# Performance work log

Hardware: AMD Instinct MI355X
Metric: run time of the kernel (lower is better)

## Reference

```python
import jax, jax.numpy as jnp
import numpy as np

L, B, H, S, V, D = 2, 128, 1024, 512, 32000, 64
W_SCALE = 0.02

def setup_inputs() -> dict:
    key = jax.random.key(0)
    ks = jax.random.split(key, 17)
    f = lambda k, shape: jax.random.normal(k, shape, dtype=jnp.float32)
    return {
        "input_ids": jax.random.randint(ks[0], (1, B), 0, V),
        "h": f(ks[1], (L, B, H)),
        "c": f(ks[2], (L, B, H)),
        "h_s": f(ks[3], (S, B, H)),
        "emb": f(ks[4], (V, H)),
        "W_pt": f(ks[5], (H, H)) * W_SCALE,
        "b_pt": f(ks[6], (H,)) * W_SCALE,
        "v_pt": f(ks[7], (H,)) * W_SCALE,
        "b_v": f(ks[8], (1,)) * W_SCALE,
        "W_a": f(ks[9], (H, H)) * W_SCALE,
        "b_a": f(ks[10], (1,)) * W_SCALE,
        "W_ih": f(ks[11], (L, 4 * H, H)) * W_SCALE,
        "W_hh": f(ks[12], (L, 4 * H, H)) * W_SCALE,
        "b_ih": f(ks[13], (L, 4 * H)) * W_SCALE,
        "b_hh": f(ks[14], (L, 4 * H)) * W_SCALE,
        "W_out": f(ks[15], (V, H)) * W_SCALE,
        "b_out": f(ks[16], (V,)) * W_SCALE,
    }


def reference(input_ids, h, c, h_s, emb, W_pt, b_pt, v_pt, b_v, W_a, b_a,
              W_ih, W_hh, b_ih, b_hh, W_out, b_out):
    S_len = h_s.shape[0]
    x_emb = emb[input_ids]                     # [1, B, H]
    h_top = h[-1]                              # [B, H] top-layer decoder state
    # predicted alignment position p_t = S * sigmoid(v . tanh(W h + b))
    p_t = S_len * jax.nn.sigmoid(jnp.tanh(h_top @ W_pt.T + b_pt) @ v_pt + b_v[0])  # [B]
    s = jnp.clip(jnp.round(p_t).astype(jnp.int32), D, S_len - 1 - D)               # [B]
    # gather local window h_s[s-D : s+D+1] per batch element
    idx = s[:, None] + jnp.arange(-D, D + 1)    # [B, 2D+1]
    h_s_b = jnp.transpose(h_s, (1, 0, 2))       # [B, S, H]
    h_loc = jnp.take_along_axis(h_s_b, idx[:, :, None], axis=1)  # [B, 2D+1, H]
    # bilinear score h_t^T W_a h_s_j per window position
    scores = jnp.einsum('bh,hk,bjk->bj', h_top, W_a, h_loc) + b_a[0]  # [B, 2D+1]
    sigma2 = (D / 2.0) ** 2
    gauss = jnp.exp(-((idx.astype(p_t.dtype) - p_t[:, None]) ** 2) / (2.0 * sigma2))
    a_t = jax.nn.softmax(scores, axis=-1) * gauss                      # [B, 2D+1]
    context = jnp.einsum('bj,bjh->bh', a_t, h_loc)                     # [B, H]
    # inject context into the LSTM hidden state, then run one step
    h_in = h + context[None]                    # [L, B, H]
    x = x_emb[0]                                # [B, H]
    hs, cs = [], []
    for l in range(h.shape[0]):
        gates = x @ W_ih[l].T + b_ih[l] + h_in[l] @ W_hh[l].T + b_hh[l]
        i, f, g, o = jnp.split(gates, 4, axis=-1)
        c_new = jax.nn.sigmoid(f) * c[l] + jax.nn.sigmoid(i) * jnp.tanh(g)
        h_new = jax.nn.sigmoid(o) * jnp.tanh(c_new)
        hs.append(h_new)
        cs.append(c_new)
        x = h_new
    h_out = jnp.stack(hs)                       # [L, B, H]
    c_out = jnp.stack(cs)                       # [L, B, H]
    logits = jax.nn.log_softmax(x @ W_out.T + b_out, axis=-1)  # [B, V]
    return logits, h_out, c_out, context, s
```

## Files before the change

### kernel.cpp

```cpp
#include <hip/hip_runtime.h>
#include <hip/hip_bf16.h>
#include <math.h>

typedef __bf16 bf16_8 __attribute__((ext_vector_type(8)));
typedef __bf16 bf16_4 __attribute__((ext_vector_type(4)));
typedef float  f32x4  __attribute__((ext_vector_type(4)));

static __device__ __forceinline__ float sigmoidf_(float x){ return 1.0f/(1.0f + expf(-x)); }

#define BB 128
#define HH 1024
#define SS 512
#define VV 32000

#define OFF_A0    0u
#define OFF_A1    524288u
#define OFF_ALOG  1048576u
#define OFF_AH    1310720u
#define OFF_AM    1572864u
#define OFF_AL    1835008u
#define OFF_WAT   2097152u
#define OFF_Q     6291456u
#define OFF_Z     6815744u
#define OFF_PT    7340032u
#define OFF_SI    7340544u
#define OFF_SC    7341056u
#define OFF_G0P   7408640u
#define OFF_G1P   15797248u
#define OFF_PMAX  24185856u
#define OFF_PSUM  24313856u

__global__ void k_prep_all(const float* __restrict__ W_a, float* __restrict__ WaT,
                           const int* __restrict__ ids, const float* __restrict__ emb,
                           const float* __restrict__ h, const float* __restrict__ b_pt,
                           __bf16* __restrict__ A0, __bf16* __restrict__ Ah,
                           __bf16* __restrict__ Am, __bf16* __restrict__ Al,
                           float* __restrict__ z, float* __restrict__ q){
  __shared__ float tsm[32][33];
  int blk = blockIdx.x, t = threadIdx.x;
  if (blk < 1024){
    int kt = blk & 31, nt = blk >> 5;
    int c = t & 31, r0 = t >> 5;
    #pragma unroll
    for (int i = 0; i < 4; ++i){
      int r = r0 + 8*i;
      tsm[r][c] = W_a[(size_t)(kt*32 + r)*HH + nt*32 + c];
    }
    __syncthreads();
    #pragma unroll
    for (int i = 0; i < 4; ++i){
      int r = r0 + 8*i;
      WaT[(size_t)(nt*32 + r)*HH + kt*32 + c] = tsm[c][r];
    }
  } else {
    int b = blk - 1024, c = t*4;
    int tok = ids[b];
    f32x4 e = *(const f32x4*)(emb + (size_t)tok*HH + c);
    bf16_4 e4;
    #pragma unroll
    for (int i=0;i<4;i++) e4[i] = (__bf16)e[i];
    *(bf16_4*)(A0 + (size_t)b*2048 + c) = e4;
    f32x4 x = *(const f32x4*)(h + (size_t)BB*HH + (size_t)b*HH + c);
    bf16_4 hi4, mi4, lo4;
    #pragma unroll
    for (int i=0;i<4;i++){
      float v = x[i];
      __bf16 bh = (__bf16)v; float r1 = v - (float)bh;
      __bf16 bm = (__bf16)r1; float r2 = r1 - (float)bm;
      hi4[i]=bh; mi4[i]=bm; lo4[i]=(__bf16)r2;
    }
    *(bf16_4*)(Ah + (size_t)b*HH + c) = hi4;
    *(bf16_4*)(Am + (size_t)b*HH + c) = mi4;
    *(bf16_4*)(Al + (size_t)b*HH + c) = lo4;
    *(f32x4*)(z + (size_t)b*HH + c) = *(const f32x4*)(b_pt + c);
    *(f32x4*)(q + (size_t)b*HH + c) = f32x4{0.f,0.f,0.f,0.f};
  }
}

template<int PREC>
__device__ __forceinline__ void gemm_small(
    char* smem,
    const __bf16* __restrict__ Ah, const __bf16* __restrict__ Am, const __bf16* __restrict__ Al,
    int lda, const float* __restrict__ B1, int K,
    float* __restrict__ C, int N, int xblk, int ysplit)
{
  constexpr int NS   = PREC;
  constexpr int BK   = 32;
  constexpr int KG   = BK/8;
  constexpr int TILE = 128*BK*2;
  constexpr int UPT  = (128*KG)/256;
  char* sA = smem;
  char* sB = smem + NS*TILE;

  const int t = threadIdx.x;
  const int lane = t & 63, wave = t >> 6;
  const int wm = wave >> 1, wn = wave & 1;
  const int quad = lane >> 4, ln = lane & 15;
  const int nblock = xblk * 128;
  const int kchunk = K / ysplit;
  const int kstart = blockIdx.y * kchunk;
  const int kend = kstart + kchunk;

  f32x4 acc[4][4];
  #pragma unroll
  for (int i=0;i<4;i++)
    #pragma unroll
    for (int j=0;j<4;j++) acc[i][j] = f32x4{0.f,0.f,0.f,0.f};

  for (int k0 = kstart; k0 < kend; k0 += BK){
    #pragma unroll
    for (int i = 0; i < UPT; ++i){
      int u = t + 256*i;
      int row = u / KG, kg = u % KG;
      int sl = row*(BK*2) + (((kg ^ (row & (KG-1)))) << 4);
      *(uint4*)(sA + sl) = *(const uint4*)(Ah + (size_t)row*lda + k0 + kg*8);
      if constexpr (PREC >= 2)
        *(uint4*)(sA + TILE + sl) = *(const uint4*)(Am + (size_t)row*lda + k0 + kg*8);
      if constexpr (PREC >= 3)
        *(uint4*)(sA + 2*TILE + sl) = *(const uint4*)(Al + (size_t)row*lda + k0 + kg*8);
      int ng = nblock + row;
      const float* src = B1 + (size_t)ng*K + k0 + kg*8;
      f32x4 x0 = *(const f32x4*)(src);
      f32x4 x1 = *(const f32x4*)(src + 4);
      bf16_8 hi, mi, lo;
      #pragma unroll
      for (int qv=0;qv<8;qv++){
        float v = (qv<4) ? x0[qv] : x1[qv-4];
        __bf16 bh = (__bf16)v;
        hi[qv] = bh;
        float r1 = v - (float)bh;
        __bf16 bm = (__bf16)r1;
        mi[qv] = bm;
        lo[qv] = (__bf16)(r1 - (float)bm);
      }
      *(bf16_8*)(sB + sl) = hi;
      if constexpr (PREC >= 2) *(bf16_8*)(sB + TILE + sl) = mi;
      if constexpr (PREC >= 3) *(bf16_8*)(sB + 2*TILE + sl) = lo;
    }
    __syncthreads();
    {
      bf16_8 af[NS][4], bfr[NS][4];
      #pragma unroll
      for (int mt=0; mt<4; ++mt){
        int row = wm*64 + mt*16 + ln;
        int kg = quad;
        int sl = row*(BK*2) + (((kg ^ (row & (KG-1)))) << 4);
        #pragma unroll
        for (int s=0;s<NS;s++) af[s][mt] = *(const bf16_8*)(sA + s*TILE + sl);
      }
      #pragma unroll
      for (int nt=0; nt<4; ++nt){
        int row = wn*64 + nt*16 + ln;
        int kg = quad;
        int sl = row*(BK*2) + (((kg ^ (row & (KG-1)))) << 4);
        #pragma unroll
        for (int s=0;s<NS;s++) bfr[s][nt] = *(const bf16_8*)(sB + s*TILE + sl);
      }
      #pragma unroll
      for (int mt=0; mt<4; ++mt)
        #pragma unroll
        for (int nt=0; nt<4; ++nt){
          acc[mt][nt] = __builtin_amdgcn_mfma_f32_16x16x32_bf16(af[0][mt], bfr[0][nt], acc[mt][nt], 0,0,0);
          if constexpr (PREC >= 2){
            acc[mt][nt] = __builtin_amdgcn_mfma_f32_16x16x32_bf16(af[0][mt], bfr[1][nt], acc[mt][nt], 0,0,0);
            acc[mt][nt] = __builtin_amdgcn_mfma_f32_16x16x32_bf16(af[1][mt], bfr[0][nt], acc[mt][nt], 0,0,0);
          }
          if constexpr (PREC >= 3){
            acc[mt][nt] = __builtin_amdgcn_mfma_f32_16x16x32_bf16(af[0][mt], bfr[2][nt], acc[mt][nt], 0,0,0);
            acc[mt][nt] = __builtin_amdgcn_mfma_f32_16x16x32_bf16(af[1][mt], bfr[1][nt], acc[mt][nt], 0,0,0);
            acc[mt][nt] = __builtin_amdgcn_mfma_f32_16x16x32_bf16(af[2][mt], bfr[0][nt], acc[mt][nt], 0,0,0);
          }
        }
    }
    __syncthreads();
  }

  #pragma unroll
  for (int nt=0; nt<4; ++nt){
    int n = nblock + wn*64 + nt*16 + ln;
    #pragma unroll
    for (int mt=0; mt<4; ++mt){
      int m0 = wm*64 + mt*16 + quad*4;
      #pragma unroll
      for (int r=0;r<4;++r)
        atomicAdd(C + (size_t)(m0 + r)*N + n, acc[mt][nt][r]);
    }
  }
}

__global__ __launch_bounds__(256) void k_qz(
    const __bf16* __restrict__ Ah, const __bf16* __restrict__ Am, const __bf16* __restrict__ Al,
    const float* __restrict__ WaT, const float* __restrict__ Wpt,
    float* __restrict__ q, float* __restrict__ z)
{
  __shared__ __align__(16) char smem[49152];
  if (blockIdx.x < 8)
    gemm_small<2>(smem, Ah, Am, nullptr, 1024, WaT, 1024, q, 1024, blockIdx.x, 4);
  else
    gemm_small<3>(smem, Ah, Am, Al, 1024, Wpt, 1024, z, 1024, blockIdx.x - 8, 4);
}

template<int PREC, int EPI>
__global__ __launch_bounds__(256) void k_gemm(
    const __bf16* __restrict__ Ah, const __bf16* __restrict__ Am, const __bf16* __restrict__ Al,
    int lda,
    const float* __restrict__ B1, const float* __restrict__ B2, int K1, int K2,
    const float* __restrict__ bias,
    float* __restrict__ C, int N,
    float* __restrict__ Pmax, float* __restrict__ Psum)
{
  constexpr int BK  = 64;
  constexpr int KG  = BK/8;
  constexpr int TILE = 128*BK*2;
  constexpr int UPT = (128*KG)/256;
  __shared__ __align__(16) char smem[2*TILE];
  char* sA = smem;
  char* sB = smem + TILE;

  const int t = threadIdx.x;
  const int lane = t & 63, wave = t >> 6;
  const int wm = wave >> 1, wn = wave & 1;
  const int quad = lane >> 4, ln = lane & 15;
  const int nblock = blockIdx.x * 128;
  const int K = K1 + K2;
  const int kchunk = K / gridDim.y;
  const int kstart = blockIdx.y * kchunk;
  const int kend = kstart + kchunk;

  f32x4 acc[4][4];
  #pragma unroll
  for (int i=0;i<4;i++)
    #pragma unroll
    for (int j=0;j<4;j++) acc[i][j] = f32x4{0.f,0.f,0.f,0.f};

  uint4 aR[UPT]; f32x4 bR[UPT][2];
  auto issue = [&](int k0){
    #pragma unroll
    for (int i=0;i<UPT;++i){
      int u = t + 256*i, row = u/KG, kg = u%KG;
      aR[i] = *(const uint4*)(Ah + (size_t)row*lda + k0 + kg*8);
      int ng = nblock + row;
      const float* src = (k0 < K1) ? (B1 + (size_t)ng*K1 + k0 + kg*8)
                                   : (B2 + (size_t)ng*K2 + (k0 - K1) + kg*8);
      bR[i][0] = *(const f32x4*)(src);
      bR[i][1] = *(const f32x4*)(src + 4);
    }
  };
  issue(kstart);
  for (int k0 = kstart; k0 < kend; k0 += BK){
    __syncthreads();
    #pragma unroll
    for (int i=0;i<UPT;++i){
      int u = t + 256*i, row = u/KG, kg = u%KG;
      int sl = row*(BK*2) + (((kg ^ (row & (KG-1)))) << 4);
      *(uint4*)(sA + sl) = aR[i];
      bf16_8 hi;
      #pragma unroll
      for (int qv=0;qv<8;++qv) hi[qv] = (__bf16)((qv<4) ? bR[i][0][qv] : bR[i][1][qv-4]);
      *(bf16_8*)(sB + sl) = hi;
    }
    __syncthreads();
    if (k0 + BK < kend) issue(k0 + BK);
    #pragma unroll
    for (int ks = 0; ks < BK/32; ++ks){
      bf16_8 af[4], bfr[4];
      #pragma unroll
      for (int mt=0; mt<4; ++mt){
        int row = wm*64 + mt*16 + ln;
        int kg = ks*4 + quad;
        int sl = row*(BK*2) + (((kg ^ (row & (KG-1)))) << 4);
        af[mt] = *(const bf16_8*)(sA + sl);
      }
      #pragma unroll
      for (int nt=0; nt<4; ++nt){
        int row = wn*64 + nt*16 + ln;
        int kg = ks*4 + quad;
        int sl = row*(BK*2) + (((kg ^ (row & (KG-1)))) << 4);
        bfr[nt] = *(const bf16_8*)(sB + sl);
      }
      #pragma unroll
      for (int mt=0; mt<4; ++mt)
        #pragma unroll
        for (int nt=0; nt<4; ++nt)
          acc[mt][nt] = __builtin_amdgcn_mfma_f32_16x16x32_bf16(af[mt], bfr[nt], acc[mt][nt], 0,0,0);
    }
  }

  if constexpr (EPI == 4){
    float* Cp = C + (size_t)blockIdx.y * 128 * N;
    #pragma unroll
    for (int nt=0; nt<4; ++nt){
      int n = nblock + wn*64 + nt*16 + ln;
      #pragma unroll
      for (int mt=0; mt<4; ++mt){
        int m0 = wm*64 + mt*16 + quad*4;
        #pragma unroll
        for (int r=0;r<4;++r)
          Cp[(size_t)(m0 + r)*N + n] = acc[mt][nt][r];
      }
    }
  } else if constexpr (EPI == 2){
    __syncthreads();
    float* redm = (float*)smem;
    float* reds = (float*)smem + 256;
    float rmax[16];
    #pragma unroll
    for (int mt=0; mt<4; ++mt)
      #pragma unroll
      for (int r=0;r<4;++r){
        float m4 = -1e30f;
        #pragma unroll
        for (int nt=0;nt<4;++nt){
          int n = nblock + wn*64 + nt*16 + ln;
          m4 = fmaxf(m4, acc[mt][nt][r] + bias[n]);
        }
        #pragma unroll
        for (int m=1;m<16;m<<=1) m4 = fmaxf(m4, __shfl_xor(m4, m));
        rmax[mt*4+r] = m4;
      }
    if (ln == 0){
      #pragma unroll
      for (int mt=0;mt<4;++mt)
        #pragma unroll
        for (int r=0;r<4;++r)
          redm[wn*128 + wm*64 + mt*16 + quad*4 + r] = rmax[mt*4+r];
    }
    __syncthreads();
    #pragma unroll
    for (int mt=0; mt<4; ++mt)
      #pragma unroll
      for (int r=0;r<4;++r){
        int row = wm*64 + mt*16 + quad*4 + r;
        float M = fmaxf(redm[row], redm[128 + row]);
        float s4 = 0.f;
        #pragma unroll
        for (int nt=0;nt<4;++nt){
          int n = nblock + wn*64 + nt*16 + ln;
          float v = acc[mt][nt][r] + bias[n];
          C[(size_t)row*N + n] = v;
          s4 += expf(v - M);
        }
        #pragma unroll
        for (int m=1;m<16;m<<=1) s4 += __shfl_xor(s4, m);
        if (ln == 0) reds[wn*128 + row] = s4;
      }
    __syncthreads();
    if (wn == 0 && ln == 0){
      #pragma unroll
      for (int mt=0;mt<4;++mt)
        #pragma unroll
        for (int r=0;r<4;++r){
          int row = wm*64 + mt*16 + quad*4 + r;
          float M = fmaxf(redm[row], redm[128 + row]);
          Pmax[(size_t)blockIdx.x*128 + row] = M;
          Psum[(size_t)blockIdx.x*128 + row] = reds[row] + reds[128 + row];
        }
    }
  }
}

__global__ __launch_bounds__(256) void k_scores(
    const float* __restrict__ z, const float* __restrict__ v_pt, const float* __restrict__ b_v,
    const float* __restrict__ q, const float* __restrict__ h_s,
    const float* __restrict__ b_a,
    float* __restrict__ sc, float* __restrict__ p_t, int* __restrict__ s_i,
    float* __restrict__ out_s)
{
  __shared__ float red[4];
  __shared__ float sh[2];
  int b = blockIdx.x, t = threadIdx.x;
  {
    f32x4 zv = *(const f32x4*)(z + (size_t)b*HH + t*4);
    f32x4 vv = *(const f32x4*)(v_pt + t*4);
    float ps = tanhf(zv[0])*vv[0] + tanhf(zv[1])*vv[1] + tanhf(zv[2])*vv[2] + tanhf(zv[3])*vv[3];
    #pragma unroll
    for (int m=1;m<64;m<<=1) ps += __shfl_xor(ps, m);
    if ((t&63)==0) red[t>>6] = ps;
    __syncthreads();
    if (t == 0){
      float tot = red[0]+red[1]+red[2]+red[3] + b_v[0];
      float p = (float)SS * sigmoidf_(tot);
      float sf = rintf(p);
      sf = fminf(fmaxf(sf, 64.0f), 447.0f);
      sh[0] = p; sh[1] = sf;
      if (blockIdx.y == 0){ p_t[b] = p; s_i[b] = (int)sf; out_s[b] = sf; }
    }
    __syncthreads();
  }
  int si = (int)sh[1];
  int jj = blockIdx.y*4 + (t >> 6);
  if (jj >= 129) return;
  int lane = t & 63;
  int pos = si - 64 + jj;
  const float* row = h_s + ((size_t)pos*BB + b)*HH;
  const float* qb  = q + (size_t)b*HH;
  f32x4 a = f32x4{0.f,0.f,0.f,0.f};
  #pragma unroll
  for (int c = lane*4; c < HH; c += 256){
    f32x4 r4 = *(const f32x4*)(row + c);
    f32x4 q4 = *(const f32x4*)(qb + c);
    a += r4*q4;
  }
  float sdot = a[0]+a[1]+a[2]+a[3];
  #pragma unroll
  for (int m=1;m<64;m<<=1) sdot += __shfl_xor(sdot, m);
  if (lane == 0) sc[b*132 + jj] = sdot + b_a[0];
}

__global__ __launch_bounds__(256) void k_context(
    const float* __restrict__ sc, const int* __restrict__ s_i, const float* __restrict__ p_t,
    const float* __restrict__ h_s, const float* __restrict__ h,
    float* __restrict__ ctx_out, __bf16* __restrict__ A0, __bf16* __restrict__ A1){
  __shared__ float sat[132];
  __shared__ float sctx[4][512];
  __shared__ int spos;
  int bb = blockIdx.x;
  int b = bb >> 1, half = bb & 1;
  int t = threadIdx.x, w = t >> 6, l = t & 63;
  if (w == 0){
    const float* scb = sc + b*132;
    float mx = -1e30f;
    for (int j=l; j<129; j+=64) mx = fmaxf(mx, scb[j]);
    #pragma unroll
    for (int m=1;m<64;m<<=1) mx = fmaxf(mx, __shfl_xor(mx, m));
    float sum = 0.f;
    for (int j=l; j<129; j+=64) sum += expf(scb[j] - mx);
    #pragma unroll
    for (int m=1;m<64;m<<=1) sum += __shfl_xor(sum, m);
    float inv = 1.0f/sum;
    float pt = p_t[b];
    int si = s_i[b];
    if (l == 0) spos = si - 64;
    float s0 = (float)(si - 64);
    for (int j=l; j<129; j+=64){
      float e = expf(scb[j]-mx)*inv;
      float d = (s0 + (float)j) - pt;
      sat[j] = e * expf(-(d*d) * (1.0f/2048.0f));
    }
  }
  __syncthreads();
  int pos0 = spos;
  int jstart = (w == 0) ? 0 : (33 + 32*(w-1));
  int jcnt   = (w == 0) ? 33 : 32;
  const float* base = h_s + ((size_t)pos0*BB + b)*HH + half*512;
  f32x4 acc0 = f32x4{0.f,0.f,0.f,0.f};
  f32x4 acc1 = f32x4{0.f,0.f,0.f,0.f};
  for (int j = jstart; j < jstart + jcnt; ++j){
    const float* row = base + (size_t)j*BB*HH;
    float aj = sat[j];
    acc0 += *(const f32x4*)(row + l*4) * aj;
    acc1 += *(const f32x4*)(row + 256 + l*4) * aj;
  }
  *(f32x4*)(&sctx[w][l*4])       = acc0;
  *(f32x4*)(&sctx[w][256 + l*4]) = acc1;
  __syncthreads();
  if (t < 128){
    int c = t*4;
    f32x4 v = *(f32x4*)(&sctx[0][c]) + *(f32x4*)(&sctx[1][c])
            + *(f32x4*)(&sctx[2][c]) + *(f32x4*)(&sctx[3][c]);
    int gc = half*512 + c;
    *(f32x4*)(ctx_out + (size_t)b*HH + gc) = v;
    f32x4 h0 = *(const f32x4*)(h + (size_t)b*HH + gc) + v;
    f32x4 h1 = *(const f32x4*)(h + (size_t)BB*HH + (size_t)b*HH + gc) + v;
    bf16_4 v0, v1;
    #pragma unroll
    for (int i=0;i<4;i++){ v0[i]=(__bf16)h0[i]; v1[i]=(__bf16)h1[i]; }
    *(bf16_4*)(A0 + (size_t)b*2048 + 1024 + gc) = v0;
    *(bf16_4*)(A1 + (size_t)b*2048 + 1024 + gc) = v1;
  }
}

__global__ void k_cell(const float* __restrict__ part,
                       const float* __restrict__ bih, const float* __restrict__ bhh,
                       const float* __restrict__ c_in,
                       float* __restrict__ h_out, float* __restrict__ c_out,
                       __bf16* __restrict__ Anext, int strideNext){
  int g = blockIdx.x*256 + threadIdx.x;
  int b = g >> 10, hc = g & 1023;
  float ig = bih[hc]        + bhh[hc];
  float fg = bih[1024 + hc] + bhh[1024 + hc];
  float gg = bih[2048 + hc] + bhh[2048 + hc];
  float og = bih[3072 + hc] + bhh[3072 + hc];
  #pragma unroll
  for (int y = 0; y < 4; ++y){
    const float* gb = part + ((size_t)y*BB + b)*4096;
    ig += gb[hc]; fg += gb[1024+hc]; gg += gb[2048+hc]; og += gb[3072+hc];
  }
  float cn = sigmoidf_(fg)*c_in[g] + sigmoidf_(ig)*tanhf(gg);
  float hn = sigmoidf_(og)*tanhf(cn);
  c_out[g] = cn; h_out[g] = hn;
  Anext[(size_t)b*strideNext + hc] = (__bf16)hn;
}

__global__ void k_lsesub(const float* __restrict__ Pmax, const float* __restrict__ Psum,
                         float* __restrict__ out){
  int b = blockIdx.y, l = threadIdx.x;
  float M = -1e30f;
  for (int i=l; i<250; i+=64) M = fmaxf(M, Pmax[(size_t)i*128 + b]);
  #pragma unroll
  for (int m=1;m<64;m<<=1) M = fmaxf(M, __shfl_xor(M, m));
  float s = 0.f;
  for (int i=l; i<250; i+=64) s += Psum[(size_t)i*128 + b] * expf(Pmax[(size_t)i*128 + b] - M);
  #pragma unroll
  for (int m=1;m<64;m<<=1) s += __shfl_xor(s, m);
  float L = M + logf(s);
  int i = blockIdx.x*256 + l*4;
  f32x4 v = *(f32x4*)(out + (size_t)b*VV + i);
  v[0]-=L; v[1]-=L; v[2]-=L; v[3]-=L;
  *(f32x4*)(out + (size_t)b*VV + i) = v;
}

extern "C" void kernel_launch(void* const* d_in, const int* in_sizes, int n_in,
                              void* d_out, int out_size, void* d_ws, size_t ws_size,
                              hipStream_t stream){
  const int*   ids   = (const int*)d_in[0];
  const float* h     = (const float*)d_in[1];
  const float* c     = (const float*)d_in[2];
  const float* h_s   = (const float*)d_in[3];
  const float* emb   = (const float*)d_in[4];
  const float* W_pt  = (const float*)d_in[5];
  const float* b_pt  = (const float*)d_in[6];
  const float* v_pt  = (const float*)d_in[7];
  const float* b_v   = (const float*)d_in[8];
  const float* W_a   = (const float*)d_in[9];
  const float* b_a   = (const float*)d_in[10];
  const float* W_ih  = (const float*)d_in[11];
  const float* W_hh  = (const float*)d_in[12];
  const float* b_ih  = (const float*)d_in[13];
  const float* b_hh  = (const float*)d_in[14];
  const float* W_out = (const float*)d_in[15];
  const float* b_out = (const float*)d_in[16];

  char* ws = (char*)d_ws;
  __bf16* A0   = (__bf16*)(ws + OFF_A0);
  __bf16* A1   = (__bf16*)(ws + OFF_A1);
  __bf16* Alog = (__bf16*)(ws + OFF_ALOG);
  __bf16* Ah   = (__bf16*)(ws + OFF_AH);
  __bf16* Am   = (__bf16*)(ws + OFF_AM);
  __bf16* Al   = (__bf16*)(ws + OFF_AL);
  float* WaT   = (float*)(ws + OFF_WAT);
  float* q     = (float*)(ws + OFF_Q);
  float* z     = (float*)(ws + OFF_Z);
  float* p_t   = (float*)(ws + OFF_PT);
  int*   s_i   = (int*)  (ws + OFF_SI);
  float* sc    = (float*)(ws + OFF_SC);
  float* g0p   = (float*)(ws + OFF_G0P);
  float* g1p   = (float*)(ws + OFF_G1P);
  float* Pmax  = (float*)(ws + OFF_PMAX);
  float* Psum  = (float*)(ws + OFF_PSUM);

  float* out        = (float*)d_out;
  float* out_logits = out;
  float* out_h      = out + 4096000;
  float* out_c      = out + 4358144;
  float* out_ctx    = out + 4620288;
  float* out_s      = out + 4751360;

  k_prep_all<<<1152, 256, 0, stream>>>(W_a, WaT, ids, emb, h, b_pt, A0, Ah, Am, Al, z, q);
  k_qz<<<dim3(16,4), 256, 0, stream>>>(Ah, Am, Al, WaT, W_pt, q, z);
  k_scores<<<dim3(128,33), 256, 0, stream>>>(z, v_pt, b_v, q, h_s, b_a, sc, p_t, s_i, out_s);
  k_context<<<256, 256, 0, stream>>>(sc, s_i, p_t, h_s, h, out_ctx, A0, A1);
  k_gemm<1,4><<<dim3(32,4), 256, 0, stream>>>(A0, nullptr, nullptr, 2048, W_ih, W_hh, 1024, 1024,
                                              nullptr, g0p, 4096, nullptr, nullptr);
  k_cell<<<512, 256, 0, stream>>>(g0p, b_ih, b_hh, c, out_h, out_c, A1, 2048);
  k_gemm<1,4><<<dim3(32,4), 256, 0, stream>>>(A1, nullptr, nullptr, 2048, W_ih + 4194304, W_hh + 4194304,
                                              1024, 1024, nullptr, g1p, 4096, nullptr, nullptr);
  k_cell<<<512, 256, 0, stream>>>(g1p, b_ih + 4096, b_hh + 4096, c + 131072,
                                  out_h + 131072, out_c + 131072, Alog, 1024);
  k_gemm<1,2><<<dim3(250,1), 256, 0, stream>>>(Alog, nullptr, nullptr, 1024, W_out, nullptr, 1024, 0,
                                               b_out, out_logits, 32000, Pmax, Psum);
  k_lsesub<<<dim3(125,128), 64, 0, stream>>>(Pmax, Psum, out_logits);
}
```

Baseline: 651.5 us.

## Double split-K for gate GEMMs and qz, narrow logits tiles to 64 columns

The gate GEMMs and the q/z projection now split K eight ways instead of four, and the cell kernel sums eight partials. Workspace offsets grow to hold the larger partial buffers. The logits GEMM becomes a dedicated kernel with 64-wide N tiles, launching 500 blocks instead of 250, and each wave does its own row max/sum reduction with no shared-memory cross-wave step. The aim is to fill more compute units on the MI355X for these weight-bandwidth-bound GEMMs, at the cost of more partial-sum traffic and a longer LSE reduction.

```diff
diff --git a/kernel.cpp b/kernel.cpp
--- a/kernel.cpp
+++ b/kernel.cpp
@@ -26,9 +26,9 @@
 #define OFF_SI    7340544u
 #define OFF_SC    7341056u
 #define OFF_G0P   7408640u
-#define OFF_G1P   15797248u
-#define OFF_PMAX  24185856u
-#define OFF_PSUM  24313856u
+#define OFF_G1P   24185856u
+#define OFF_PMAX  40963072u
+#define OFF_PSUM  41225216u
 
 __global__ void k_prep_all(const float* __restrict__ W_a, float* __restrict__ WaT,
                            const int* __restrict__ ids, const float* __restrict__ emb,
@@ -195,19 +195,15 @@
 {
   __shared__ __align__(16) char smem[49152];
   if (blockIdx.x < 8)
-    gemm_small<2>(smem, Ah, Am, nullptr, 1024, WaT, 1024, q, 1024, blockIdx.x, 4);
+    gemm_small<2>(smem, Ah, Am, nullptr, 1024, WaT, 1024, q, 1024, blockIdx.x, 8);
   else
-    gemm_small<3>(smem, Ah, Am, Al, 1024, Wpt, 1024, z, 1024, blockIdx.x - 8, 4);
-}
-
-template<int PREC, int EPI>
-__global__ __launch_bounds__(256) void k_gemm(
-    const __bf16* __restrict__ Ah, const __bf16* __restrict__ Am, const __bf16* __restrict__ Al,
-    int lda,
-    const float* __restrict__ B1, const float* __restrict__ B2, int K1, int K2,
-    const float* __restrict__ bias,
-    float* __restrict__ C, int N,
-    float* __restrict__ Pmax, float* __restrict__ Psum)
+    gemm_small<3>(smem, Ah, Am, Al, 1024, Wpt, 1024, z, 1024, blockIdx.x - 8, 8);
+}
+
+__global__ __launch_bounds__(256) void k_gates(
+    const __bf16* __restrict__ Ain, int lda,
+    const float* __restrict__ B1, const float* __restrict__ B2, int K1,
+    float* __restrict__ C, int N)
 {
   constexpr int BK  = 64;
   constexpr int KG  = BK/8;
@@ -222,7 +218,7 @@
   const int wm = wave >> 1, wn = wave & 1;
   const int quad = lane >> 4, ln = lane & 15;
   const int nblock = blockIdx.x * 128;
-  const int K = K1 + K2;
+  const int K = 2*K1;
   const int kchunk = K / gridDim.y;
   const int kstart = blockIdx.y * kchunk;
   const int kend = kstart + kchunk;
@@ -238,10 +234,10 @@
     #pragma unroll
     for (int i=0;i<UPT;++i){
       int u = t + 256*i, row = u/KG, kg = u%KG;
-      aR[i] = *(const uint4*)(Ah + (size_t)row*lda + k0 + kg*8);
+      aR[i] = *(const uint4*)(Ain + (size_t)row*lda + k0 + kg*8);
       int ng = nblock + row;
       const float* src = (k0 < K1) ? (B1 + (size_t)ng*K1 + k0 + kg*8)
-                                   : (B2 + (size_t)ng*K2 + (k0 - K1) + kg*8);
+                                   : (B2 + (size_t)ng*K1 + (k0 - K1) + kg*8);
       bR[i][0] = *(const f32x4*)(src);
       bR[i][1] = *(const f32x4*)(src + 4);
     }
@@ -286,77 +282,131 @@
     }
   }
 
-  if constexpr (EPI == 4){
-    float* Cp = C + (size_t)blockIdx.y * 128 * N;
-    #pragma unroll
-    for (int nt=0; nt<4; ++nt){
-      int n = nblock + wn*64 + nt*16 + ln;
-      #pragma unroll
-      for (int mt=0; mt<4; ++mt){
-        int m0 = wm*64 + mt*16 + quad*4;
+  float* Cp = C + (size_t)blockIdx.y * 128 * N;
+  #pragma unroll
+  for (int nt=0; nt<4; ++nt){
+    int n = nblock + wn*64 + nt*16 + ln;
+    #pragma unroll
+    for (int mt=0; mt<4; ++mt){
+      int m0 = wm*64 + mt*16 + quad*4;
+      #pragma unroll
+      for (int r=0;r<4;++r)
+        Cp[(size_t)(m0 + r)*N + n] = acc[mt][nt][r];
+    }
+  }
+}
+
+__global__ __launch_bounds__(256) void k_logits(
+    const __bf16* __restrict__ A, const float* __restrict__ Wout,
+    const float* __restrict__ bias, float* __restrict__ C,
+    float* __restrict__ Pmax, float* __restrict__ Psum)
+{
+  constexpr int BK = 64, KG = 8;
+  constexpr int ATILE = 128*BK*2;
+  constexpr int BTILE = 64*BK*2;
+  __shared__ __align__(16) char smem[ATILE + BTILE];
+  char* sA = smem;
+  char* sB = smem + ATILE;
+
+  const int t = threadIdx.x;
+  const int lane = t & 63, wave = t >> 6;
+  const int quad = lane >> 4, ln = lane & 15;
+  const int nblock = blockIdx.x * 64;
+
+  f32x4 acc[2][4];
+  #pragma unroll
+  for (int i=0;i<2;i++)
+    #pragma unroll
+    for (int j=0;j<4;j++) acc[i][j] = f32x4{0.f,0.f,0.f,0.f};
+
+  uint4 aR[4]; f32x4 bR[2][2];
+  auto issue = [&](int k0){
+    #pragma unroll
+    for (int i=0;i<4;++i){
+      int u = t + 256*i, row = u >> 3, kg = u & 7;
+      aR[i] = *(const uint4*)(A + (size_t)row*HH + k0 + kg*8);
+    }
+    #pragma unroll
+    for (int i=0;i<2;++i){
+      int u = t + 256*i, row = u >> 3, kg = u & 7;
+      const float* src = Wout + (size_t)(nblock + row)*HH + k0 + kg*8;
+      bR[i][0] = *(const f32x4*)(src);
+      bR[i][1] = *(const f32x4*)(src + 4);
+    }
+  };
+  issue(0);
+  for (int k0 = 0; k0 < HH; k0 += BK){
+    __syncthreads();
+    #pragma unroll
+    for (int i=0;i<4;++i){
+      int u = t + 256*i, row = u >> 3, kg = u & 7;
+      int sl = row*(BK*2) + ((kg ^ (row & 7)) << 4);
+      *(uint4*)(sA + sl) = aR[i];
+    }
+    #pragma unroll
+    for (int i=0;i<2;++i){
+      int u = t + 256*i, row = u >> 3, kg = u & 7;
+      int sl = row*(BK*2) + ((kg ^ (row & 7)) << 4);
+      bf16_8 hi;
+      #pragma unroll
+      for (int qv=0;qv<8;++qv) hi[qv] = (__bf16)((qv<4) ? bR[i][0][qv] : bR[i][1][qv-4]);
+      *(bf16_8*)(sB + sl) = hi;
+    }
+    __syncthreads();
+    if (k0 + BK < HH) issue(k0 + BK);
+    #pragma unroll
+    for (int ks = 0; ks < BK/32; ++ks){
+      bf16_8 af[2], bfr[4];
+      #pragma unroll
+      for (int mt=0; mt<2; ++mt){
+        int row = wave*32 + mt*16 + ln;
+        int kg = ks*4 + quad;
+        int sl = row*(BK*2) + ((kg ^ (row & 7)) << 4);
+        af[mt] = *(const bf16_8*)(sA + sl);
+      }
+      #pragma unroll
+      for (int nt=0; nt<4; ++nt){
+        int row = nt*16 + ln;
+        int kg = ks*4 + quad;
+        int sl = row*(BK*2) + ((kg ^ (row & 7)) << 4);
+        bfr[nt] = *(const bf16_8*)(sB + sl);
+      }
+      #pragma unroll
+      for (int mt=0; mt<2; ++mt)
         #pragma unroll
-        for (int r=0;r<4;++r)
-          Cp[(size_t)(m0 + r)*N + n] = acc[mt][nt][r];
-      }
-    }
-  } else if constexpr (EPI == 2){
-    __syncthreads();
-    float* redm = (float*)smem;
-    float* reds = (float*)smem + 256;
-    float rmax[16];
-    #pragma unroll
-    for (int mt=0; mt<4; ++mt)
-      #pragma unroll
-      for (int r=0;r<4;++r){
-        float m4 = -1e30f;
-        #pragma unroll
-        for (int nt=0;nt<4;++nt){
-          int n = nblock + wn*64 + nt*16 + ln;
-          m4 = fmaxf(m4, acc[mt][nt][r] + bias[n]);
-        }
-        #pragma unroll
-        for (int m=1;m<16;m<<=1) m4 = fmaxf(m4, __shfl_xor(m4, m));
-        rmax[mt*4+r] = m4;
-      }
-    if (ln == 0){
-      #pragma unroll
-      for (int mt=0;mt<4;++mt)
-        #pragma unroll
-        for (int r=0;r<4;++r)
-          redm[wn*128 + wm*64 + mt*16 + quad*4 + r] = rmax[mt*4+r];
-    }
-    __syncthreads();
-    #pragma unroll
-    for (int mt=0; mt<4; ++mt)
-      #pragma unroll
-      for (int r=0;r<4;++r){
-        int row = wm*64 + mt*16 + quad*4 + r;
-        float M = fmaxf(redm[row], redm[128 + row]);
-        float s4 = 0.f;
-        #pragma unroll
-        for (int nt=0;nt<4;++nt){
-          int n = nblock + wn*64 + nt*16 + ln;
-          float v = acc[mt][nt][r] + bias[n];
-          C[(size_t)row*N + n] = v;
-          s4 += expf(v - M);
-        }
-        #pragma unroll
-        for (int m=1;m<16;m<<=1) s4 += __shfl_xor(s4, m);
-        if (ln == 0) reds[wn*128 + row] = s4;
-      }
-    __syncthreads();
-    if (wn == 0 && ln == 0){
-      #pragma unroll
-      for (int mt=0;mt<4;++mt)
-        #pragma unroll
-        for (int r=0;r<4;++r){
-          int row = wm*64 + mt*16 + quad*4 + r;
-          float M = fmaxf(redm[row], redm[128 + row]);
-          Pmax[(size_t)blockIdx.x*128 + row] = M;
-          Psum[(size_t)blockIdx.x*128 + row] = reds[row] + reds[128 + row];
-        }
-    }
-  }
+        for (int nt=0; nt<4; ++nt)
+          acc[mt][nt] = __builtin_amdgcn_mfma_f32_16x16x32_bf16(af[mt], bfr[nt], acc[mt][nt], 0,0,0);
+    }
+  }
+
+  #pragma unroll
+  for (int mt=0; mt<2; ++mt)
+    #pragma unroll
+    for (int r=0; r<4; ++r){
+      int row = wave*32 + mt*16 + quad*4 + r;
+      float m4 = -1e30f;
+      #pragma unroll
+      for (int nt=0; nt<4; ++nt){
+        int n = nblock + nt*16 + ln;
+        m4 = fmaxf(m4, acc[mt][nt][r] + bias[n]);
+      }
+      #pragma unroll
+      for (int m=1;m<16;m<<=1) m4 = fmaxf(m4, __shfl_xor(m4, m));
+      float s4 = 0.f;
+      #pragma unroll
+      for (int nt=0; nt<4; ++nt){
+        int n = nblock + nt*16 + ln;
+        float v = acc[mt][nt][r] + bias[n];
+        C[(size_t)row*VV + n] = v;
+        s4 += expf(v - m4);
+      }
+      #pragma unroll
+      for (int m=1;m<16;m<<=1) s4 += __shfl_xor(s4, m);
+      if (ln == 0){
+        Pmax[(size_t)blockIdx.x*128 + row] = m4;
+        Psum[(size_t)blockIdx.x*128 + row] = s4;
+      }
+    }
 }
 
 __global__ __launch_bounds__(256) void k_scores(
@@ -482,7 +532,7 @@
   float gg = bih[2048 + hc] + bhh[2048 + hc];
   float og = bih[3072 + hc] + bhh[3072 + hc];
   #pragma unroll
-  for (int y = 0; y < 4; ++y){
+  for (int y = 0; y < 8; ++y){
     const float* gb = part + ((size_t)y*BB + b)*4096;
     ig += gb[hc]; fg += gb[1024+hc]; gg += gb[2048+hc]; og += gb[3072+hc];
   }
@@ -496,11 +546,11 @@
                          float* __restrict__ out){
   int b = blockIdx.y, l = threadIdx.x;
   float M = -1e30f;
-  for (int i=l; i<250; i+=64) M = fmaxf(M, Pmax[(size_t)i*128 + b]);
+  for (int i=l; i<500; i+=64) M = fmaxf(M, Pmax[(size_t)i*128 + b]);
   #pragma unroll
   for (int m=1;m<64;m<<=1) M = fmaxf(M, __shfl_xor(M, m));
   float s = 0.f;
-  for (int i=l; i<250; i+=64) s += Psum[(size_t)i*128 + b] * expf(Pmax[(size_t)i*128 + b] - M);
+  for (int i=l; i<500; i+=64) s += Psum[(size_t)i*128 + b] * expf(Pmax[(size_t)i*128 + b] - M);
   #pragma unroll
   for (int m=1;m<64;m<<=1) s += __shfl_xor(s, m);
   float L = M + logf(s);
@@ -557,17 +607,14 @@
   float* out_s      = out + 4751360;
 
   k_prep_all<<<1152, 256, 0, stream>>>(W_a, WaT, ids, emb, h, b_pt, A0, Ah, Am, Al, z, q);
-  k_qz<<<dim3(16,4), 256, 0, stream>>>(Ah, Am, Al, WaT, W_pt, q, z);
+  k_qz<<<dim3(16,8), 256, 0, stream>>>(Ah, Am, Al, WaT, W_pt, q, z);
   k_scores<<<dim3(128,33), 256, 0, stream>>>(z, v_pt, b_v, q, h_s, b_a, sc, p_t, s_i, out_s);
   k_context<<<256, 256, 0, stream>>>(sc, s_i, p_t, h_s, h, out_ctx, A0, A1);
-  k_gemm<1,4><<<dim3(32,4), 256, 0, stream>>>(A0, nullptr, nullptr, 2048, W_ih, W_hh, 1024, 1024,
-                                              nullptr, g0p, 4096, nullptr, nullptr);
+  k_gates<<<dim3(32,8), 256, 0, stream>>>(A0, 2048, W_ih, W_hh, 1024, g0p, 4096);
   k_cell<<<512, 256, 0, stream>>>(g0p, b_ih, b_hh, c, out_h, out_c, A1, 2048);
-  k_gemm<1,4><<<dim3(32,4), 256, 0, stream>>>(A1, nullptr, nullptr, 2048, W_ih + 4194304, W_hh + 4194304,
-                                              1024, 1024, nullptr, g1p, 4096, nullptr, nullptr);
+  k_gates<<<dim3(32,8), 256, 0, stream>>>(A1, 2048, W_ih + 4194304, W_hh + 4194304, 1024, g1p, 4096);
   k_cell<<<512, 256, 0, stream>>>(g1p, b_ih + 4096, b_hh + 4096, c + 131072,
                                   out_h + 131072, out_c + 131072, Alog, 1024);
-  k_gemm<1,2><<<dim3(250,1), 256, 0, stream>>>(Alog, nullptr, nullptr, 1024, W_out, nullptr, 1024, 0,
-                                               b_out, out_logits, 32000, Pmax, Psum);
+  k_logits<<<500, 256, 0, stream>>>(Alog, W_out, b_out, out_logits, Pmax, Psum);
   k_lsesub<<<dim3(125,128), 64, 0, stream>>>(Pmax, Psum, out_logits);
 }
```

After: 672.2 us. +3.2%, slower.
